# Performance work log

Hardware: AMD Instinct MI355X
Metric: run time of the kernel (lower is better)

Reference implementation:

```python
import jax, jax.numpy as jnp
import numpy as np

B, L, D = 4, 4096, 1024
N_HEADS = 16
HEAD_SIZE = D // N_HEADS  # 64


def setup_inputs() -> dict:
    key = jax.random.key(0)
    k_x, k_w, k_m = jax.random.split(key, 3)
    x = jax.random.normal(k_x, (B, L, D), dtype=jnp.float32)
    # nn.Linear(D, 3*head_size, bias=False): weight (3*hs, D); store transposed (D, 3*hs)
    W_qkv = jax.random.normal(k_w, (D, 3 * HEAD_SIZE), dtype=jnp.float32) * (D ** -0.5)
    attn_mask = jax.random.randint(k_m, (B, L), 0, 2).astype(jnp.bool_)
    return {"x": x, "attn_mask": attn_mask, "W_qkv": W_qkv}


def reference(x, attn_mask, W_qkv):
    # x: (B, L, D); W_qkv: (D, 3*hs); attn_mask: (B, L) True = attend
    qkv = x @ W_qkv                                # (B, L, 3*hs)
    q, k, v = jnp.split(qkv, 3, axis=-1)           # each (B, L, hs)
    scale = HEAD_SIZE ** -0.5
    scores = jnp.einsum('bqd,bkd->bqk', q, k) * scale   # (B, L, L)
    neg_inf = jnp.finfo(scores.dtype).min
    scores = jnp.where(attn_mask[:, None, :], scores, neg_inf)
    weights = jax.nn.softmax(scores, axis=-1)      # (B, L, L)
    out = jnp.einsum('bqk,bkd->bqd', weights, v)   # (B, L, hs)
    return out
```

## Files before the change

### kernel.cpp

```cpp
#include <hip/hip_runtime.h>

typedef __bf16 bf16_t;
typedef __bf16 bf16x8 __attribute__((ext_vector_type(8)));
typedef __bf16 bf16x4 __attribute__((ext_vector_type(4)));
typedef float  f32x4  __attribute__((ext_vector_type(4)));
struct uint4_t { unsigned x, y, z, w; };

#define B_  4
#define L_  4096
#define D_  1024
#define HS  64
#define NQ  192
#define SCL2E 0.1803368801111204f
#define MFMA16 __builtin_amdgcn_mfma_f32_16x16x32_bf16

__global__ __launch_bounds__(256) void pack_w_kernel(const void* __restrict__ Win,
                                                     const unsigned char* __restrict__ mask,
                                                     const unsigned short* __restrict__ xw,
                                                     bf16_t* __restrict__ Wtp,
                                                     int* __restrict__ flags) {
    __shared__ int c1, c23, cbad;
    int tid = threadIdx.x;
    if (tid == 0) { c1 = 0; c23 = 0; cbad = 0; }
    __syncthreads();
    uint4_t m[4];
#pragma unroll
    for (int i = 0; i < 4; ++i)
        m[i] = *(const uint4_t*)(mask + tid * 16 + i * 4096);
    int a = 0, bc = 0;
#pragma unroll
    for (int i = 0; i < 4; ++i) {
        const unsigned* w = (const unsigned*)&m[i];
#pragma unroll
        for (int j = 0; j < 4; ++j) {
            if (w[j] & 0x0000ff00u) a++;
            if (w[j] & 0xffff0000u) bc++;
        }
    }
    uint4_t xm = *(const uint4_t*)(xw + tid * 8);
    int bad = 0;
    const unsigned* xwv = (const unsigned*)&xm;
#pragma unroll
    for (int j = 0; j < 4; ++j)
#pragma unroll
        for (int h = 0; h < 2; ++h) {
            unsigned s = (xwv[j] >> (16 * h)) & 0xFFFFu;
            unsigned e = (s >> 7) & 0xFF;
            if (e > 150 || (e < 90 && e != 0)) bad++;
        }
    if (a)   atomicAdd(&c1, a);
    if (bc)  atomicAdd(&c23, bc);
    if (bad) atomicAdd(&cbad, bad);
    __syncthreads();
    int f32 = (cbad >= 64) ? 1 : 0;
    if (blockIdx.x == 0 && tid == 0) {
        flags[0] = (c1 > 0) ? 1 : ((c23 > 0) ? 2 : 0);
        flags[1] = f32;
    }

    int idx = blockIdx.x * 256 + tid;
    int lane = idx & 63;
    int t    = (idx >> 6) & 3;
    int kc   = (idx >> 8) & 31;
    int ct   = idx >> 13;
    int n  = ct * 64 + t * 16 + (lane & 15);
    int k0 = kc * 32 + (lane >> 4) * 8;
    bf16x8 v;
#pragma unroll
    for (int j = 0; j < 8; ++j) {
        if (f32) v[j] = (bf16_t)(((const float*)Win)[(k0 + j) * NQ + n]);
        else     v[j] = ((const bf16_t*)Win)[(k0 + j) * NQ + n];
    }
    *(bf16x8*)(Wtp + (size_t)idx * 8) = v;
}

__global__ __launch_bounds__(256, 2) void qkv_gemm_kernel(const void* __restrict__ xin,
                                                          const int* __restrict__ flags,
                                                          const bf16_t* __restrict__ Wtp,
                                                          bf16_t* __restrict__ Qb,
                                                          bf16_t* __restrict__ Kb,
                                                          bf16_t* __restrict__ Vt) {
    __shared__ __align__(16) bf16_t xs[32 * 520];
    __shared__ __align__(16) bf16_t sqk[32 * 136];
    __shared__ __align__(16) bf16_t sv[64 * 40];

    int tid = threadIdx.x;
    int wave = tid >> 6, lane = tid & 63, quad = lane >> 4, l16 = lane & 15;
    int rg = wave & 1, ch = wave >> 1;
    int m0 = blockIdx.x * 32;
    int xf = flags[1];

    f32x4 acc[6] = {};
    bf16x8 Ba[6], Bb[6];

    auto stage = [&](int h) {
        bf16x8 tmp[8];
#pragma unroll
        for (int j = 0; j < 8; ++j) {
            int c = tid + j * 256;
            int row = c >> 6, off = (c & 63) * 8;
            if (xf) {
                const float* xp = (const float*)xin + (size_t)(m0 + row) * D_ + h * 512 + off;
                f32x4 lo = *(const f32x4*)xp, hi = *(const f32x4*)(xp + 4);
                tmp[j][0] = (bf16_t)lo[0]; tmp[j][1] = (bf16_t)lo[1];
                tmp[j][2] = (bf16_t)lo[2]; tmp[j][3] = (bf16_t)lo[3];
                tmp[j][4] = (bf16_t)hi[0]; tmp[j][5] = (bf16_t)hi[1];
                tmp[j][6] = (bf16_t)hi[2]; tmp[j][7] = (bf16_t)hi[3];
            } else {
                tmp[j] = *(const bf16x8*)((const bf16_t*)xin + (size_t)(m0 + row) * D_ + h * 512 + off);
            }
        }
#pragma unroll
        for (int j = 0; j < 8; ++j) {
            int c = tid + j * 256;
            int row = c >> 6, off = (c & 63) * 8;
            *(bf16x8*)&xs[row * 520 + off] = tmp[j];
        }
    };
    auto loadB6 = [&](int ks, bf16x8* Bv) {
#pragma unroll
        for (int i = 0; i < 6; ++i) {
            int st = ch * 6 + i, ct2 = st >> 2, tt = st & 3;
            Bv[i] = *(const bf16x8*)(Wtp + ((size_t)(ct2 * 32 + ks) * 4 + tt) * 512 + lane * 8);
        }
    };
    auto compute6 = [&](int ks, const bf16x8* Bv) {
        bf16x8 A = *(const bf16x8*)&xs[(rg * 16 + l16) * 520 + (ks & 15) * 32 + quad * 8];
#pragma unroll
        for (int i = 0; i < 6; ++i)
            acc[i] = MFMA16(A, Bv[i], acc[i], 0, 0, 0);
    };

    stage(0);
    loadB6(0, Ba);
    __syncthreads();
#pragma unroll
    for (int half = 0; half < 2; ++half) {
        int base = half * 16;
        for (int m = 0; m < 16; m += 2) {
            int ks = base + m;
            loadB6(ks + 1, Bb);
            compute6(ks, Ba);
            loadB6(ks + 2 <= 31 ? ks + 2 : 31, Ba);
            compute6(ks + 1, Bb);
        }
        if (half == 0) {
            __syncthreads();
            stage(1);
            __syncthreads();
        }
    }

    int rowb = rg * 16 + quad * 4;
#pragma unroll
    for (int i = 0; i < 6; ++i) {
        int col = ch * 96 + i * 16 + l16;
#pragma unroll
        for (int r = 0; r < 4; ++r) {
            bf16_t hv = (bf16_t)acc[i][r];
            if (col < 128) sqk[(rowb + r) * 136 + col] = hv;
            else           sv[(col - 128) * 40 + rowb + r] = hv;
        }
    }
    __syncthreads();

    int bb = m0 >> 12, l0 = m0 & 4095;
#pragma unroll
    for (int it = 0; it < 2; ++it) {
        int c = tid + it * 256;
        int row = c >> 4, off = (c & 15) * 8;
        bf16x8 v = *(const bf16x8*)&sqk[row * 136 + off];
        if (off < 64) *(bf16x8*)(Qb + (size_t)(bb * L_ + l0 + row) * HS + off) = v;
        else          *(bf16x8*)(Kb + (size_t)(bb * L_ + l0 + row) * HS + off - 64) = v;
    }
    {
        int d = tid >> 2, off = (tid & 3) * 8;
        bf16x8 v = *(const bf16x8*)&sv[d * 40 + off];
        *(bf16x8*)(Vt + (size_t)(bb * HS + d) * L_ + l0 + off) = v;
    }
}

template<int NSPLIT>
__global__ __launch_bounds__(256, 4) void attn_kernel(const bf16_t* __restrict__ Qb,
                                                      const bf16_t* __restrict__ Kb,
                                                      const bf16_t* __restrict__ Vt,
                                                      const void* __restrict__ maskp,
                                                      const int* __restrict__ flags,
                                                      float* __restrict__ Opart,
                                                      float* __restrict__ lpart,
                                                      void* __restrict__ outv) {
    constexpr int KCH = L_ / NSPLIT;
    constexpr int NIT = KCH / 64;
    __shared__ __align__(16) bf16_t ktile[2][64 * 72];
    __shared__ __align__(16) bf16_t plds[4][32 * 72];
    __shared__ float mb[KCH];

    int tid = threadIdx.x, wave = tid >> 6, lane = tid & 63;
    int quad = lane >> 4, l16 = lane & 15;
    int grp = blockIdx.x % (B_ * NSPLIT);
    int qt  = blockIdx.x / (B_ * NSPLIT);
    int s = grp / B_, b = grp % B_;
    int q0 = qt * 128;
    int kbase = s * KCH;

    const float NEGINF = -__builtin_inff();
    int mkind = flags[0];
    if (mkind == 1) {
        const unsigned char* mp = (const unsigned char*)maskp + b * L_ + kbase;
        for (int i = tid; i < KCH; i += 256) mb[i] = mp[i] ? 0.0f : NEGINF;
    } else if (mkind == 2) {
        const float* mp = (const float*)maskp + b * L_ + kbase;
        for (int i = tid; i < KCH; i += 256) mb[i] = (mp[i] != 0.0f) ? 0.0f : NEGINF;
    } else {
        const int* mp = (const int*)maskp + b * L_ + kbase;
        for (int i = tid; i < KCH; i += 256) mb[i] = mp[i] ? 0.0f : NEGINF;
    }

    bf16x8 aQ[2][2];
#pragma unroll
    for (int rg = 0; rg < 2; ++rg) {
        const bf16_t* qp = Qb + (size_t)(b * L_ + q0 + wave * 32 + rg * 16 + l16) * HS + quad * 8;
        aQ[rg][0] = *(const bf16x8*)qp;
        aQ[rg][1] = *(const bf16x8*)(qp + 32);
    }
    bf16x8 ones;
#pragma unroll
    for (int j = 0; j < 8; ++j) ones[j] = (bf16_t)1.0f;

    const bf16_t* Kbase = Kb + (size_t)b * L_ * HS;
    const bf16_t* Vbase = Vt + (size_t)b * HS * L_;

    f32x4 O[2][4] = {};
    f32x4 O5[2] = {};
    bf16_t* pw = &plds[wave][0];
    bf16x8 kr[2];

    auto kstage_load = [&](int t) {
#pragma unroll
        for (int j = 0; j < 2; ++j) {
            int c = tid + j * 256;
            int row = c >> 3, off = (c & 7) * 8;
            kr[j] = *(const bf16x8*)(Kbase + (size_t)(kbase + t * 64 + row) * HS + off);
        }
    };
    auto kstage_store = [&](int buf) {
#pragma unroll
        for (int j = 0; j < 2; ++j) {
            int c = tid + j * 256;
            int row = c >> 3, off = (c & 7) * 8;
            *(bf16x8*)&ktile[buf][row * 72 + off] = kr[j];
        }
    };

    kstage_load(0);
    kstage_store(0);
    __syncthreads();

    for (int t = 0; t < NIT; ++t) {
        int kb = kbase + t * 64;
        bool more = (t + 1 < NIT);
        if (more) kstage_load(t + 1);

        bf16x8 V0[4];
#pragma unroll
        for (int nt = 0; nt < 4; ++nt)
            V0[nt] = *(const bf16x8*)(Vbase + (size_t)(nt * 16 + l16) * L_ + kb + quad * 8);

        const bf16_t* kl = &ktile[t & 1][0];
#pragma unroll
        for (int h = 0; h < 2; ++h) {
            f32x4 sc[2][2];
#pragma unroll
            for (int s2 = 0; s2 < 2; ++s2) {
                int st = h * 2 + s2;
                bf16x8 kb0 = *(const bf16x8*)&kl[(st * 16 + l16) * 72 + quad * 8];
                bf16x8 kb1 = *(const bf16x8*)&kl[(st * 16 + l16) * 72 + 32 + quad * 8];
#pragma unroll
                for (int rg = 0; rg < 2; ++rg) {
                    f32x4 t0 = {};
                    t0 = MFMA16(aQ[rg][0], kb0, t0, 0, 0, 0);
                    t0 = MFMA16(aQ[rg][1], kb1, t0, 0, 0, 0);
                    sc[rg][s2] = t0;
                }
            }
#pragma unroll
            for (int s2 = 0; s2 < 2; ++s2) {
                int st = h * 2 + s2;
                float bl = mb[t * 64 + st * 16 + l16];
#pragma unroll
                for (int rg = 0; rg < 2; ++rg)
#pragma unroll
                    for (int r = 0; r < 4; ++r) {
                        float p = exp2f(fmaf(sc[rg][s2][r], SCL2E, bl));
                        pw[(rg * 16 + quad * 4 + r) * 72 + st * 16 + l16] = (bf16_t)p;
                    }
            }
        }

#pragma unroll
        for (int rg = 0; rg < 2; ++rg) {
            bf16x8 aP = *(const bf16x8*)&pw[(rg * 16 + l16) * 72 + quad * 8];
#pragma unroll
            for (int nt = 0; nt < 4; ++nt)
                O[rg][nt] = MFMA16(aP, V0[nt], O[rg][nt], 0, 0, 0);
            O5[rg] = MFMA16(aP, ones, O5[rg], 0, 0, 0);
        }
        bf16x8 V1[4];
#pragma unroll
        for (int nt = 0; nt < 4; ++nt)
            V1[nt] = *(const bf16x8*)(Vbase + (size_t)(nt * 16 + l16) * L_ + kb + 32 + quad * 8);
#pragma unroll
        for (int rg = 0; rg < 2; ++rg) {
            bf16x8 aP = *(const bf16x8*)&pw[(rg * 16 + l16) * 72 + 32 + quad * 8];
#pragma unroll
            for (int nt = 0; nt < 4; ++nt)
                O[rg][nt] = MFMA16(aP, V1[nt], O[rg][nt], 0, 0, 0);
            O5[rg] = MFMA16(aP, ones, O5[rg], 0, 0, 0);
        }

        if (more) kstage_store((t + 1) & 1);
        __syncthreads();
    }

    int of32 = flags[1];
#pragma unroll
    for (int rg = 0; rg < 2; ++rg)
#pragma unroll
        for (int r = 0; r < 4; ++r) {
            float sm = O5[rg][r];
            int row = q0 + wave * 32 + rg * 16 + quad * 4 + r;
            if (NSPLIT == 1) {
                float inv = 1.0f / sm;
                size_t base = (size_t)(b * L_ + row) * HS;
                if (of32) {
                    float* op = (float*)outv + base;
#pragma unroll
                    for (int nt = 0; nt < 4; ++nt) op[nt * 16 + l16] = O[rg][nt][r] * inv;
                } else {
                    bf16_t* op = (bf16_t*)outv + base;
#pragma unroll
                    for (int nt = 0; nt < 4; ++nt) op[nt * 16 + l16] = (bf16_t)(O[rg][nt][r] * inv);
                }
            } else {
                float* op = Opart + (size_t)s * (B_ * L_ * HS) + (size_t)(b * L_ + row) * HS;
#pragma unroll
                for (int nt = 0; nt < 4; ++nt) op[nt * 16 + l16] = O[rg][nt][r];
                if (l16 == 0) lpart[(size_t)s * (B_ * L_) + b * L_ + row] = sm;
            }
        }
}

__global__ __launch_bounds__(256) void reduce_kernel(const float* __restrict__ Opart,
                                                     const float* __restrict__ lpart,
                                                     const int* __restrict__ flags,
                                                     void* __restrict__ outv,
                                                     int nsplit) {
    int i4 = (blockIdx.x * 256 + threadIdx.x) * 4;
    int row = i4 >> 6;
    f32x4 acc = {};
    float lsum = 0.f;
    for (int s = 0; s < nsplit; ++s) {
        acc  += *(const f32x4*)&Opart[(size_t)s * (B_ * L_ * HS) + i4];
        lsum += lpart[(size_t)s * (B_ * L_) + row];
    }
    float inv = 1.0f / lsum;
    if (flags[1]) {
        f32x4 r = { acc[0] * inv, acc[1] * inv, acc[2] * inv, acc[3] * inv };
        *(f32x4*)&((float*)outv)[i4] = r;
    } else {
        bf16x4 r;
#pragma unroll
        for (int j = 0; j < 4; ++j) r[j] = (bf16_t)(acc[j] * inv);
        *(bf16x4*)&((bf16_t*)outv)[i4] = r;
    }
}

extern "C" void kernel_launch(void* const* d_in, const int* in_sizes, int n_in,
                              void* d_out, int out_size, void* d_ws, size_t ws_size,
                              hipStream_t stream) {
    (void)in_sizes; (void)n_in; (void)out_size;
    const void* x    = d_in[0];
    const void* mask = d_in[1];
    const void* W    = d_in[2];

    char* ws = (char*)d_ws;
    bf16_t* Qb    = (bf16_t*)(ws);
    bf16_t* Kb    = (bf16_t*)(ws + (2u << 20));
    bf16_t* Vt    = (bf16_t*)(ws + (4u << 20));
    bf16_t* Wtp   = (bf16_t*)(ws + (6u << 20));
    int*    flags = (int*)   (ws + (6u << 20) + (512u << 10));
    float*  Opart = (float*) (ws + (7u << 20));

    auto need = [](int ns) -> size_t {
        return (7u << 20) + (size_t)ns * (B_ * L_ * HS * 4)
                          + (size_t)ns * (B_ * L_ * 4) + 4096;
    };
    int nsplit = (ws_size >= need(8)) ? 8 : (ws_size >= need(4)) ? 4 : 1;
    float* lpart = (float*)(ws + (7u << 20) + (size_t)nsplit * (B_ * L_ * HS * 4));

    pack_w_kernel<<<96, 256, 0, stream>>>(W, (const unsigned char*)mask,
                                          (const unsigned short*)x, Wtp, flags);
    qkv_gemm_kernel<<<512, 256, 0, stream>>>(x, flags, Wtp, Qb, Kb, Vt);
    if (nsplit == 8) {
        attn_kernel<8><<<32 * B_ * 8, 256, 0, stream>>>(Qb, Kb, Vt, mask, flags,
                                                        Opart, lpart, d_out);
        reduce_kernel<<<(B_ * L_ * HS) / 1024, 256, 0, stream>>>(Opart, lpart, flags,
                                                                 d_out, 8);
    } else if (nsplit == 4) {
        attn_kernel<4><<<32 * B_ * 4, 256, 0, stream>>>(Qb, Kb, Vt, mask, flags,
                                                        Opart, lpart, d_out);
        reduce_kernel<<<(B_ * L_ * HS) / 1024, 256, 0, stream>>>(Opart, lpart, flags,
                                                                 d_out, 4);
    } else {
        attn_kernel<1><<<32 * B_, 256, 0, stream>>>(Qb, Kb, Vt, mask, flags,
                                                    Opart, lpart, d_out);
    }
}
```

Before: 167.3 us.

## Drop LDS staging in QKV GEMM and shrink attention LDS footprint

The QKV projection kernel no longer stages x through a large shared-memory tile. Each wave now loads its A fragments straight from global memory and covers both row groups for 48 output columns, and the launch bound is raised to 4 blocks per SM. In the attention kernel the K tile padding is cut from 72 to 68, and the per-wave P buffer is halved by interleaving the softmax and PV MFMA per 32-key half. This lowers register and LDS pressure so occupancy can rise. The cost is redundant global x loads across the four waves and possible LDS bank conflicts with the new strides.

```diff
diff --git a/kernel.cpp b/kernel.cpp
--- a/kernel.cpp
+++ b/kernel.cpp
@@ -74,92 +74,82 @@
     *(bf16x8*)(Wtp + (size_t)idx * 8) = v;
 }
 
-__global__ __launch_bounds__(256, 2) void qkv_gemm_kernel(const void* __restrict__ xin,
+__global__ __launch_bounds__(256, 4) void qkv_gemm_kernel(const void* __restrict__ xin,
                                                           const int* __restrict__ flags,
                                                           const bf16_t* __restrict__ Wtp,
                                                           bf16_t* __restrict__ Qb,
                                                           bf16_t* __restrict__ Kb,
                                                           bf16_t* __restrict__ Vt) {
-    __shared__ __align__(16) bf16_t xs[32 * 520];
     __shared__ __align__(16) bf16_t sqk[32 * 136];
     __shared__ __align__(16) bf16_t sv[64 * 40];
 
     int tid = threadIdx.x;
     int wave = tid >> 6, lane = tid & 63, quad = lane >> 4, l16 = lane & 15;
-    int rg = wave & 1, ch = wave >> 1;
+    int ch = wave;
     int m0 = blockIdx.x * 32;
     int xf = flags[1];
 
     f32x4 acc[6] = {};
-    bf16x8 Ba[6], Bb[6];
-
-    auto stage = [&](int h) {
-        bf16x8 tmp[8];
-#pragma unroll
-        for (int j = 0; j < 8; ++j) {
-            int c = tid + j * 256;
-            int row = c >> 6, off = (c & 63) * 8;
-            if (xf) {
-                const float* xp = (const float*)xin + (size_t)(m0 + row) * D_ + h * 512 + off;
+    bf16x8 Aa[2], Ab[2], Ba[3], Bb[3];
+
+    const bf16_t* xb   = (const bf16_t*)xin;
+    const float*  xb32 = (const float*)xin;
+    size_t rowoff0 = (size_t)(m0 + l16) * D_;
+    size_t rowoff1 = (size_t)(m0 + 16 + l16) * D_;
+
+    auto loadA = [&](int ks, bf16x8* Av) {
+        int k0 = ks * 32 + quad * 8;
+        if (xf) {
+#pragma unroll
+            for (int rg = 0; rg < 2; ++rg) {
+                const float* xp = xb32 + (rg ? rowoff1 : rowoff0) + k0;
                 f32x4 lo = *(const f32x4*)xp, hi = *(const f32x4*)(xp + 4);
-                tmp[j][0] = (bf16_t)lo[0]; tmp[j][1] = (bf16_t)lo[1];
-                tmp[j][2] = (bf16_t)lo[2]; tmp[j][3] = (bf16_t)lo[3];
-                tmp[j][4] = (bf16_t)hi[0]; tmp[j][5] = (bf16_t)hi[1];
-                tmp[j][6] = (bf16_t)hi[2]; tmp[j][7] = (bf16_t)hi[3];
-            } else {
-                tmp[j] = *(const bf16x8*)((const bf16_t*)xin + (size_t)(m0 + row) * D_ + h * 512 + off);
-            }
-        }
-#pragma unroll
-        for (int j = 0; j < 8; ++j) {
-            int c = tid + j * 256;
-            int row = c >> 6, off = (c & 63) * 8;
-            *(bf16x8*)&xs[row * 520 + off] = tmp[j];
-        }
-    };
-    auto loadB6 = [&](int ks, bf16x8* Bv) {
-#pragma unroll
-        for (int i = 0; i < 6; ++i) {
-            int st = ch * 6 + i, ct2 = st >> 2, tt = st & 3;
+                Av[rg][0] = (bf16_t)lo[0]; Av[rg][1] = (bf16_t)lo[1];
+                Av[rg][2] = (bf16_t)lo[2]; Av[rg][3] = (bf16_t)lo[3];
+                Av[rg][4] = (bf16_t)hi[0]; Av[rg][5] = (bf16_t)hi[1];
+                Av[rg][6] = (bf16_t)hi[2]; Av[rg][7] = (bf16_t)hi[3];
+            }
+        } else {
+            Av[0] = *(const bf16x8*)(xb + rowoff0 + k0);
+            Av[1] = *(const bf16x8*)(xb + rowoff1 + k0);
+        }
+    };
+    auto loadB = [&](int ks, bf16x8* Bv) {
+#pragma unroll
+        for (int i = 0; i < 3; ++i) {
+            int st = ch * 3 + i, ct2 = st >> 2, tt = st & 3;
             Bv[i] = *(const bf16x8*)(Wtp + ((size_t)(ct2 * 32 + ks) * 4 + tt) * 512 + lane * 8);
         }
     };
-    auto compute6 = [&](int ks, const bf16x8* Bv) {
-        bf16x8 A = *(const bf16x8*)&xs[(rg * 16 + l16) * 520 + (ks & 15) * 32 + quad * 8];
-#pragma unroll
-        for (int i = 0; i < 6; ++i)
-            acc[i] = MFMA16(A, Bv[i], acc[i], 0, 0, 0);
-    };
-
-    stage(0);
-    loadB6(0, Ba);
-    __syncthreads();
-#pragma unroll
-    for (int half = 0; half < 2; ++half) {
-        int base = half * 16;
-        for (int m = 0; m < 16; m += 2) {
-            int ks = base + m;
-            loadB6(ks + 1, Bb);
-            compute6(ks, Ba);
-            loadB6(ks + 2 <= 31 ? ks + 2 : 31, Ba);
-            compute6(ks + 1, Bb);
-        }
-        if (half == 0) {
-            __syncthreads();
-            stage(1);
-            __syncthreads();
-        }
-    }
-
-    int rowb = rg * 16 + quad * 4;
-#pragma unroll
-    for (int i = 0; i < 6; ++i) {
-        int col = ch * 96 + i * 16 + l16;
-#pragma unroll
-        for (int r = 0; r < 4; ++r) {
-            bf16_t hv = (bf16_t)acc[i][r];
-            if (col < 128) sqk[(rowb + r) * 136 + col] = hv;
-            else           sv[(col - 128) * 40 + rowb + r] = hv;
+    auto mm = [&](const bf16x8* Av, const bf16x8* Bv) {
+#pragma unroll
+        for (int i = 0; i < 3; ++i)
+#pragma unroll
+            for (int rg = 0; rg < 2; ++rg)
+                acc[rg * 3 + i] = MFMA16(Av[rg], Bv[i], acc[rg * 3 + i], 0, 0, 0);
+    };
+
+    loadA(0, Aa); loadB(0, Ba);
+    for (int ks = 0; ks < 32; ks += 2) {
+        loadA(ks + 1, Ab); loadB(ks + 1, Bb);
+        mm(Aa, Ba);
+        int kn = (ks + 2 < 32) ? ks + 2 : 31;
+        loadA(kn, Aa); loadB(kn, Ba);
+        mm(Ab, Bb);
+    }
+
+#pragma unroll
+    for (int i = 0; i < 3; ++i) {
+        int col = ch * 48 + i * 16 + l16;
+#pragma unroll
+        for (int rg = 0; rg < 2; ++rg) {
+            int rowb = rg * 16 + quad * 4;
+#pragma unroll
+            for (int r = 0; r < 4; ++r) {
+                bf16_t hv = (bf16_t)acc[rg * 3 + i][r];
+                if (col < 128) sqk[(rowb + r) * 136 + col] = hv;
+                else           sv[(col - 128) * 40 + rowb + r] = hv;
+            }
         }
     }
     __syncthreads();
@@ -191,8 +181,8 @@
                                                       void* __restrict__ outv) {
     constexpr int KCH = L_ / NSPLIT;
     constexpr int NIT = KCH / 64;
-    __shared__ __align__(16) bf16_t ktile[2][64 * 72];
-    __shared__ __align__(16) bf16_t plds[4][32 * 72];
+    __shared__ __align__(16) bf16_t ktile[2][64 * 68];
+    __shared__ __align__(16) bf16_t plds[4][32 * 36];
     __shared__ float mb[KCH];
 
     int tid = threadIdx.x, wave = tid >> 6, lane = tid & 63;
@@ -248,7 +238,7 @@
         for (int j = 0; j < 2; ++j) {
             int c = tid + j * 256;
             int row = c >> 3, off = (c & 7) * 8;
-            *(bf16x8*)&ktile[buf][row * 72 + off] = kr[j];
+            *(bf16x8*)&ktile[buf][row * 68 + off] = kr[j];
         }
     };
 
@@ -261,20 +251,20 @@
         bool more = (t + 1 < NIT);
         if (more) kstage_load(t + 1);
 
-        bf16x8 V0[4];
-#pragma unroll
-        for (int nt = 0; nt < 4; ++nt)
-            V0[nt] = *(const bf16x8*)(Vbase + (size_t)(nt * 16 + l16) * L_ + kb + quad * 8);
-
         const bf16_t* kl = &ktile[t & 1][0];
 #pragma unroll
         for (int h = 0; h < 2; ++h) {
+            bf16x8 V[4];
+#pragma unroll
+            for (int nt = 0; nt < 4; ++nt)
+                V[nt] = *(const bf16x8*)(Vbase + (size_t)(nt * 16 + l16) * L_ + kb + h * 32 + quad * 8);
+
             f32x4 sc[2][2];
 #pragma unroll
             for (int s2 = 0; s2 < 2; ++s2) {
                 int st = h * 2 + s2;
-                bf16x8 kb0 = *(const bf16x8*)&kl[(st * 16 + l16) * 72 + quad * 8];
-                bf16x8 kb1 = *(const bf16x8*)&kl[(st * 16 + l16) * 72 + 32 + quad * 8];
+                bf16x8 kb0 = *(const bf16x8*)&kl[(st * 16 + l16) * 68 + quad * 8];
+                bf16x8 kb1 = *(const bf16x8*)&kl[(st * 16 + l16) * 68 + 32 + quad * 8];
 #pragma unroll
                 for (int rg = 0; rg < 2; ++rg) {
                     f32x4 t0 = {};
@@ -285,37 +275,23 @@
             }
 #pragma unroll
             for (int s2 = 0; s2 < 2; ++s2) {
-                int st = h * 2 + s2;
-                float bl = mb[t * 64 + st * 16 + l16];
+                float bl = mb[t * 64 + (h * 2 + s2) * 16 + l16];
 #pragma unroll
                 for (int rg = 0; rg < 2; ++rg)
 #pragma unroll
                     for (int r = 0; r < 4; ++r) {
                         float p = exp2f(fmaf(sc[rg][s2][r], SCL2E, bl));
-                        pw[(rg * 16 + quad * 4 + r) * 72 + st * 16 + l16] = (bf16_t)p;
+                        pw[(rg * 16 + quad * 4 + r) * 36 + s2 * 16 + l16] = (bf16_t)p;
                     }
             }
-        }
-
-#pragma unroll
-        for (int rg = 0; rg < 2; ++rg) {
-            bf16x8 aP = *(const bf16x8*)&pw[(rg * 16 + l16) * 72 + quad * 8];
-#pragma unroll
-            for (int nt = 0; nt < 4; ++nt)
-                O[rg][nt] = MFMA16(aP, V0[nt], O[rg][nt], 0, 0, 0);
-            O5[rg] = MFMA16(aP, ones, O5[rg], 0, 0, 0);
-        }
-        bf16x8 V1[4];
-#pragma unroll
-        for (int nt = 0; nt < 4; ++nt)
-            V1[nt] = *(const bf16x8*)(Vbase + (size_t)(nt * 16 + l16) * L_ + kb + 32 + quad * 8);
-#pragma unroll
-        for (int rg = 0; rg < 2; ++rg) {
-            bf16x8 aP = *(const bf16x8*)&pw[(rg * 16 + l16) * 72 + 32 + quad * 8];
-#pragma unroll
-            for (int nt = 0; nt < 4; ++nt)
-                O[rg][nt] = MFMA16(aP, V1[nt], O[rg][nt], 0, 0, 0);
-            O5[rg] = MFMA16(aP, ones, O5[rg], 0, 0, 0);
+#pragma unroll
+            for (int rg = 0; rg < 2; ++rg) {
+                bf16x8 aP = *(const bf16x8*)&pw[(rg * 16 + l16) * 36 + quad * 8];
+#pragma unroll
+                for (int nt = 0; nt < 4; ++nt)
+                    O[rg][nt] = MFMA16(aP, V[nt], O[rg][nt], 0, 0, 0);
+                O5[rg] = MFMA16(aP, ones, O5[rg], 0, 0, 0);
+            }
         }
 
         if (more) kstage_store((t + 1) & 1);
```

Result: slower. 200.4 us (+19.8%).

## Pre-swizzle K tiles in GEMM epilogue and stream them via global_load_lds

Applied to the files above, without the earlier changes.

The QKV GEMM now writes K in a tiled, XOR-swizzled layout of 64-row tiles, so each tile is contiguous in global memory. The attention kernel copies those tiles straight into LDS with global_load_lds (direct DMA), replacing the register round-trip load/store staging and the padded 72-stride tile. The XOR swizzle is meant to avoid LDS bank conflicts without padding, and the change frees the VGPRs that held staged K. The risk is the async LDS write relying on the single barrier per iteration for ordering, with no explicit vmcnt wait before the tile is read.

```diff
diff --git a/kernel.cpp b/kernel.cpp
--- a/kernel.cpp
+++ b/kernel.cpp
@@ -5,6 +5,9 @@
 typedef __bf16 bf16x4 __attribute__((ext_vector_type(4)));
 typedef float  f32x4  __attribute__((ext_vector_type(4)));
 struct uint4_t { unsigned x, y, z, w; };
+
+typedef const __attribute__((address_space(1))) void gvoid_t;
+typedef __attribute__((address_space(3))) void lvoid_t;
 
 #define B_  4
 #define L_  4096
@@ -13,6 +16,10 @@
 #define NQ  192
 #define SCL2E 0.1803368801111204f
 #define MFMA16 __builtin_amdgcn_mfma_f32_16x16x32_bf16
+
+__device__ __forceinline__ void gld16(const void* g, void* l) {
+    __builtin_amdgcn_global_load_lds((gvoid_t*)g, (lvoid_t*)l, 16, 0, 0);
+}
 
 __global__ __launch_bounds__(256) void pack_w_kernel(const void* __restrict__ Win,
                                                      const unsigned char* __restrict__ mask,
@@ -78,7 +85,7 @@
                                                           const int* __restrict__ flags,
                                                           const bf16_t* __restrict__ Wtp,
                                                           bf16_t* __restrict__ Qb,
-                                                          bf16_t* __restrict__ Kb,
+                                                          bf16_t* __restrict__ Ksw,
                                                           bf16_t* __restrict__ Vt) {
     __shared__ __align__(16) bf16_t xs[32 * 520];
     __shared__ __align__(16) bf16_t sqk[32 * 136];
@@ -170,8 +177,15 @@
         int c = tid + it * 256;
         int row = c >> 4, off = (c & 15) * 8;
         bf16x8 v = *(const bf16x8*)&sqk[row * 136 + off];
-        if (off < 64) *(bf16x8*)(Qb + (size_t)(bb * L_ + l0 + row) * HS + off) = v;
-        else          *(bf16x8*)(Kb + (size_t)(bb * L_ + l0 + row) * HS + off - 64) = v;
+        if (off < 64) {
+            *(bf16x8*)(Qb + (size_t)(bb * L_ + l0 + row) * HS + off) = v;
+        } else {
+            int l = l0 + row;
+            int g = (off >> 3) - 8;
+            int gp = g ^ (l & 7);
+            *(bf16x8*)(Ksw + (size_t)(bb * 64 + (l >> 6)) * 4096
+                           + (size_t)(l & 63) * 64 + gp * 8) = v;
+        }
     }
     {
         int d = tid >> 2, off = (tid & 3) * 8;
@@ -182,7 +196,7 @@
 
 template<int NSPLIT>
 __global__ __launch_bounds__(256, 4) void attn_kernel(const bf16_t* __restrict__ Qb,
-                                                      const bf16_t* __restrict__ Kb,
+                                                      const bf16_t* __restrict__ Ksw,
                                                       const bf16_t* __restrict__ Vt,
                                                       const void* __restrict__ maskp,
                                                       const int* __restrict__ flags,
@@ -191,7 +205,7 @@
                                                       void* __restrict__ outv) {
     constexpr int KCH = L_ / NSPLIT;
     constexpr int NIT = KCH / 64;
-    __shared__ __align__(16) bf16_t ktile[2][64 * 72];
+    __shared__ __align__(16) bf16_t ktile[2][64 * 64];
     __shared__ __align__(16) bf16_t plds[4][32 * 72];
     __shared__ float mb[KCH];
 
@@ -202,6 +216,18 @@
     int s = grp / B_, b = grp % B_;
     int q0 = qt * 128;
     int kbase = s * KCH;
+
+    const bf16_t* Ktiles = Ksw + (size_t)(b * 64 + (kbase >> 6)) * 4096;
+    auto kdma = [&](int t, int buf) {
+        const bf16_t* g = Ktiles + (size_t)t * 4096;
+#pragma unroll
+        for (int j = 0; j < 2; ++j) {
+            int cbase = wave * 64 + j * 256;
+            gld16(g + (size_t)(cbase + lane) * 8, &ktile[buf][cbase * 8]);
+        }
+    };
+
+    kdma(0, 0);
 
     const float NEGINF = -__builtin_inff();
     int mkind = flags[0];
@@ -227,39 +253,22 @@
 #pragma unroll
     for (int j = 0; j < 8; ++j) ones[j] = (bf16_t)1.0f;
 
-    const bf16_t* Kbase = Kb + (size_t)b * L_ * HS;
     const bf16_t* Vbase = Vt + (size_t)b * HS * L_;
 
     f32x4 O[2][4] = {};
     f32x4 O5[2] = {};
     bf16_t* pw = &plds[wave][0];
-    bf16x8 kr[2];
-
-    auto kstage_load = [&](int t) {
-#pragma unroll
-        for (int j = 0; j < 2; ++j) {
-            int c = tid + j * 256;
-            int row = c >> 3, off = (c & 7) * 8;
-            kr[j] = *(const bf16x8*)(Kbase + (size_t)(kbase + t * 64 + row) * HS + off);
-        }
-    };
-    auto kstage_store = [&](int buf) {
-#pragma unroll
-        for (int j = 0; j < 2; ++j) {
-            int c = tid + j * 256;
-            int row = c >> 3, off = (c & 7) * 8;
-            *(bf16x8*)&ktile[buf][row * 72 + off] = kr[j];
-        }
-    };
-
-    kstage_load(0);
-    kstage_store(0);
+
+    int rph = l16 & 7;
+    int g0 = (quad ^ rph) * 8;
+    int g1 = ((quad + 4) ^ rph) * 8;
+
     __syncthreads();
 
     for (int t = 0; t < NIT; ++t) {
         int kb = kbase + t * 64;
         bool more = (t + 1 < NIT);
-        if (more) kstage_load(t + 1);
+        if (more) kdma(t + 1, (t + 1) & 1);
 
         bf16x8 V0[4];
 #pragma unroll
@@ -273,8 +282,9 @@
 #pragma unroll
             for (int s2 = 0; s2 < 2; ++s2) {
                 int st = h * 2 + s2;
-                bf16x8 kb0 = *(const bf16x8*)&kl[(st * 16 + l16) * 72 + quad * 8];
-                bf16x8 kb1 = *(const bf16x8*)&kl[(st * 16 + l16) * 72 + 32 + quad * 8];
+                int rbase = (st * 16 + l16) * 64;
+                bf16x8 kb0 = *(const bf16x8*)&kl[rbase + g0];
+                bf16x8 kb1 = *(const bf16x8*)&kl[rbase + g1];
 #pragma unroll
                 for (int rg = 0; rg < 2; ++rg) {
                     f32x4 t0 = {};
@@ -318,7 +328,6 @@
             O5[rg] = MFMA16(aP, ones, O5[rg], 0, 0, 0);
         }
 
-        if (more) kstage_store((t + 1) & 1);
         __syncthreads();
     }
 
@@ -385,7 +394,7 @@
 
     char* ws = (char*)d_ws;
     bf16_t* Qb    = (bf16_t*)(ws);
-    bf16_t* Kb    = (bf16_t*)(ws + (2u << 20));
+    bf16_t* Ksw   = (bf16_t*)(ws + (2u << 20));
     bf16_t* Vt    = (bf16_t*)(ws + (4u << 20));
     bf16_t* Wtp   = (bf16_t*)(ws + (6u << 20));
     int*    flags = (int*)   (ws + (6u << 20) + (512u << 10));
@@ -400,19 +409,19 @@
 
     pack_w_kernel<<<96, 256, 0, stream>>>(W, (const unsigned char*)mask,
                                           (const unsigned short*)x, Wtp, flags);
-    qkv_gemm_kernel<<<512, 256, 0, stream>>>(x, flags, Wtp, Qb, Kb, Vt);
+    qkv_gemm_kernel<<<512, 256, 0, stream>>>(x, flags, Wtp, Qb, Ksw, Vt);
     if (nsplit == 8) {
-        attn_kernel<8><<<32 * B_ * 8, 256, 0, stream>>>(Qb, Kb, Vt, mask, flags,
+        attn_kernel<8><<<32 * B_ * 8, 256, 0, stream>>>(Qb, Ksw, Vt, mask, flags,
                                                         Opart, lpart, d_out);
         reduce_kernel<<<(B_ * L_ * HS) / 1024, 256, 0, stream>>>(Opart, lpart, flags,
                                                                  d_out, 8);
     } else if (nsplit == 4) {
-        attn_kernel<4><<<32 * B_ * 4, 256, 0, stream>>>(Qb, Kb, Vt, mask, flags,
+        attn_kernel<4><<<32 * B_ * 4, 256, 0, stream>>>(Qb, Ksw, Vt, mask, flags,
                                                         Opart, lpart, d_out);
         reduce_kernel<<<(B_ * L_ * HS) / 1024, 256, 0, stream>>>(Opart, lpart, flags,
                                                                  d_out, 4);
     } else {
-        attn_kernel<1><<<32 * B_, 256, 0, stream>>>(Qb, Kb, Vt, mask, flags,
+        attn_kernel<1><<<32 * B_, 256, 0, stream>>>(Qb, Ksw, Vt, mask, flags,
                                                     Opart, lpart, d_out);
     }
 }
```

Result: no change. 168.6 us (+0.8%).
